# Optimization experiments

Measured on AMD Instinct MI355X. Metric: run time of the kernel, lower is better.

## Reference

```python
import jax, jax.numpy as jnp
import numpy as np
import math

DIM, H, Q_RANK, KV_RANK = 2048, 16, 768, 512
QK_STATIC, QK_ROT, V_DIM = 128, 64, 128
QK_TOTAL = QK_STATIC + QK_ROT
BS, SEQ = 2, 1024


def rmsnorm(x, scale, eps=1e-6):
    xf = x.astype(jnp.float32)
    return scale * (xf * jax.lax.rsqrt(jnp.mean(xf * xf, axis=-1, keepdims=True) + eps))


def half_rotate(x):
    h = x.shape[-1] // 2
    return jnp.concatenate([-x[..., h:], x[..., :h]], axis=-1)


def rope_tables(seq_len, dim):
    inv_freq = 1.0 / (10000.0 ** (jnp.arange(0, dim, 2, dtype=jnp.float32) / dim))
    freqs = jnp.arange(seq_len, dtype=jnp.float32)[:, None] * inv_freq[None, :]
    cos = jnp.concatenate([jnp.cos(freqs), jnp.cos(freqs)], axis=-1)  # (S, dim)
    sin = jnp.concatenate([jnp.sin(freqs), jnp.sin(freqs)], axis=-1)
    return cos, sin


def setup_inputs() -> dict:
    key = jax.random.key(0)
    ks = jax.random.split(key, 10)
    sc = lambda fan_in: 1.0 / math.sqrt(fan_in)
    x = jax.random.normal(ks[0], (BS, SEQ, DIM), dtype=jnp.float32)
    causal = jnp.where(jnp.tril(jnp.ones((SEQ, SEQ), dtype=bool)), 0.0, -1e9).astype(jnp.float32)
    mask = jnp.broadcast_to(causal[None], (BS, SEQ, SEQ))
    return {
        "x": x,
        "start_pos": 0,
        "mask": mask,
        "q_down_w": jax.random.normal(ks[1], (Q_RANK, DIM)) * sc(DIM),
        "q_down_b": jnp.zeros((Q_RANK,), jnp.float32),
        "q_norm_scale": jnp.ones((Q_RANK,), jnp.float32),
        "q_up_w": jax.random.normal(ks[2], (H * QK_TOTAL, Q_RANK)) * sc(Q_RANK),
        "q_up_b": jnp.zeros((H * QK_TOTAL,), jnp.float32),
        "kv_down_w": jax.random.normal(ks[3], (KV_RANK + QK_ROT, DIM)) * sc(DIM),
        "kv_down_b": jnp.zeros((KV_RANK + QK_ROT,), jnp.float32),
        "kv_norm_scale": jnp.ones((KV_RANK,), jnp.float32),
        "kv_up_w": jax.random.normal(ks[4], (H * (QK_STATIC + V_DIM), KV_RANK)) * sc(KV_RANK),
        "out_w": jax.random.normal(ks[5], (DIM, H * V_DIM)) * sc(H * V_DIM),
        "out_b": jnp.zeros((DIM,), jnp.float32),
    }


def reference(x, start_pos, mask, q_down_w, q_down_b, q_norm_scale, q_up_w, q_up_b,
              kv_down_w, kv_down_b, kv_norm_scale, kv_up_w, out_w, out_b):
    bs, seq_len, _ = x.shape
    # q path: down-proj -> RMSNorm -> up-proj
    q = rmsnorm(x @ q_down_w.T + q_down_b, q_norm_scale)
    q = (q @ q_up_w.T + q_up_b).reshape(bs, seq_len, H, QK_TOTAL)
    q_static, q_rot = q[..., :QK_STATIC], q[..., QK_STATIC:]
    # kv path: shared down-proj producing latent features + rotary key part
    kv = x @ kv_down_w.T + kv_down_b
    kv_feat, k_rot = kv[..., :KV_RANK], kv[..., KV_RANK:]
    # RoPE (original indexes positions 0..seq_len-1)
    cos, sin = rope_tables(seq_len, QK_ROT)
    q_rot = q_rot * cos[None, :, None, :] + half_rotate(q_rot) * sin[None, :, None, :]
    k_rot = k_rot * cos[None, :, :] + half_rotate(k_rot) * sin[None, :, :]  # (b, t, r)
    kv_normed = rmsnorm(kv_feat, kv_norm_scale)  # latent cache contents (b, t, c)
    # matrix absorption: fold kv_up key-weights into q
    w_k_abs = kv_up_w[: H * QK_STATIC, :].reshape(H, QK_STATIC, KV_RANK)
    w_v_abs = kv_up_w[-H * V_DIM :, :].reshape(H, V_DIM, KV_RANK)
    q_static_proj = jnp.einsum('bshd,hdc->bshc', q_static, w_k_abs)
    attn_scores = (jnp.einsum('bshc,btc->bsht', q_static_proj, kv_normed)
                   + jnp.einsum('bshr,btr->bsht', q_rot, k_rot)) / math.sqrt(QK_TOTAL)
    attn_scores = attn_scores + mask[:, :, None, :]
    attn_weights = jax.nn.softmax(attn_scores, axis=-1)
    # attend over latent features, then expand with absorbed value weights
    ctx_c = jnp.einsum('bsht,btc->bshc', attn_weights, kv_normed)
    ctx = jnp.einsum('bshc,hdc->bshd', ctx_c, w_v_abs)
    out = ctx.reshape(bs, seq_len, H * V_DIM) @ out_w.T + out_b
    return out
```

## Files before the change

kernel.cpp:

```cpp
#include <hip/hip_runtime.h>
#include <stdint.h>
#include <stddef.h>


typedef __attribute__((ext_vector_type(8))) short bf16x8;
typedef __attribute__((ext_vector_type(4))) float f32x4;

__device__ inline float b2f(unsigned short v){
    union { unsigned u; float f; } x; x.u = ((unsigned)v) << 16; return x.f;
}
__device__ inline unsigned short f2b(float f){
    union { float f; unsigned u; } x; x.f = f;
    unsigned r = x.u + 0x7fffu + ((x.u >> 16) & 1u);
    return (unsigned short)(r >> 16);
}

__device__ __forceinline__ void gl2lds16(const unsigned short* g, unsigned short* l){
    __builtin_amdgcn_global_load_lds(
        (__attribute__((address_space(1))) void*)const_cast<unsigned short*>(g),
        (__attribute__((address_space(3))) void*)l,
        16, 0, 0);
}

template<typename TC>
__global__ __launch_bounds__(256) void mfma_gemm_bt(
    const unsigned short* __restrict__ A, const unsigned short* __restrict__ B,
    const float* __restrict__ bias, TC* __restrict__ C,
    int M, int N, int K, int lda, int ldb, int ldc,
    int zdiv, long sA_hi, long sA_lo, long sB_hi, long sB_lo, long sC_hi, long sC_lo,
    float alpha, int causal)
{
    int z, bm, bn;
    if (causal & 4){ z = blockIdx.x; bm = blockIdx.y; bn = blockIdx.z; }
    else           { z = blockIdx.z; bm = blockIdx.y; bn = blockIdx.x; }
    int m0, n0;
    if (causal & 1){
        int i = bm;
        int mt = (int)((sqrtf(8.f * i + 1.f) - 1.f) * 0.5f);
        while ((mt + 1) * (mt + 2) / 2 <= i) ++mt;
        while (mt * (mt + 1) / 2 > i) --mt;
        n0 = (i - mt * (mt + 1) / 2) * 128;
        m0 = mt * 128;
    } else { m0 = bm * 128; n0 = bn * 128; }
    if (causal & 2) K = min(K, m0 + 128);

    __shared__ unsigned short As[3][4096];
    __shared__ unsigned short Bs[3][4096];
    const int zh = z / zdiv, zl = z % zdiv;
    A += (size_t)zh * sA_hi + (size_t)zl * sA_lo;
    B += (size_t)zh * sB_hi + (size_t)zl * sB_lo;
    C += (size_t)zh * sC_hi + (size_t)zl * sC_lo;

    const int tid = threadIdx.x, w = tid >> 6, lane = tid & 63;
    const int wm = w >> 1, wn = w & 1;

    const int srow = w * 32 + (lane >> 2);
    const int schunk = ((lane & 3) ^ ((lane >> 3) & 3)) * 8;
    const unsigned short* gA = A + (size_t)(m0 + srow) * lda + schunk;
    const unsigned short* gB = B + (size_t)(n0 + srow) * ldb + schunk;

    const int ktiles = K >> 5;
    auto stage = [&](int buf, int kt){
        const int k0 = kt << 5;
        gl2lds16(gA + k0,            &As[buf][w * 1024]);
        gl2lds16(gA + k0 + 16 * lda, &As[buf][w * 1024 + 512]);
        gl2lds16(gB + k0,            &Bs[buf][w * 1024]);
        gl2lds16(gB + k0 + 16 * ldb, &Bs[buf][w * 1024 + 512]);
    };
    stage(0, 0);
    if (ktiles > 1) stage(1, 1);

    f32x4 acc[4][4] = {};
    const int lm = lane & 15;
    const int kq = (((lane >> 4) ^ (lm >> 1)) & 3) * 8;

    int cur = 0;
    for (int kt = 0; kt < ktiles; ++kt){
        if (kt + 1 < ktiles) __builtin_amdgcn_s_waitcnt(0xF74);
        else                 __builtin_amdgcn_s_waitcnt(0xF70);
        __builtin_amdgcn_s_barrier();
        __asm__ volatile("" ::: "memory");
        if (kt + 2 < ktiles) stage(cur >= 1 ? cur - 1 : 2, kt + 2);
        bf16x8 af[4], bfr[4];
        #pragma unroll
        for (int i = 0; i < 4; ++i)
            af[i] = *(const bf16x8*)&As[cur][(wm * 64 + i * 16 + lm) * 32 + kq];
        #pragma unroll
        for (int j = 0; j < 4; ++j)
            bfr[j] = *(const bf16x8*)&Bs[cur][(wn * 64 + j * 16 + lm) * 32 + kq];
        #pragma unroll
        for (int i = 0; i < 4; ++i)
            #pragma unroll
            for (int j = 0; j < 4; ++j)
                acc[i][j] = __builtin_amdgcn_mfma_f32_16x16x32_bf16(af[i], bfr[j], acc[i][j], 0, 0, 0);
        __asm__ volatile("" ::: "memory");
        cur = (cur == 2) ? 0 : cur + 1;
    }

    #pragma unroll
    for (int i = 0; i < 4; ++i){
        const int m = m0 + wm * 64 + i * 16 + (lane >> 4) * 4;
        #pragma unroll
        for (int j = 0; j < 4; ++j){
            const int n = n0 + wn * 64 + j * 16 + lm;
            if (n < N){
                const float bb = bias ? bias[n] : 0.f;
                #pragma unroll
                for (int r = 0; r < 4; ++r){
                    float v = acc[i][j][r] * alpha + bb;
                    if ((causal & 1) && n > m + r) v = -1e9f;
                    if constexpr (sizeof(TC) == 2)
                        C[(size_t)(m + r) * ldc + n] = (TC)f2b(v);
                    else
                        C[(size_t)(m + r) * ldc + n] = (TC)v;
                }
            }
        }
    }
}

__global__ __launch_bounds__(256) void flash_attn(
    const unsigned short* __restrict__ qu,
    const unsigned short* __restrict__ khcat,
    const unsigned short* __restrict__ vhT,
    unsigned short* __restrict__ ctx)
{
    const int z = blockIdx.x;
    const int mt = 15 - (int)blockIdx.y;
    const int b = z >> 4, h = z & 15;
    const int m0 = mt * 64;
    const int nkt = (mt >> 1) + 1;

    __shared__ char smem[74240];
    unsigned short (*Qs)[4096] = (unsigned short (*)[4096])smem;
    unsigned short (*Ks)[8192] = (unsigned short (*)[8192])(smem + 24576);
    unsigned short* Ps = (unsigned short*)(smem + 24576);
    float* lrow = (float*)(smem + 73728);

    const unsigned short* kB = khcat + (size_t)z * 196608;
    const unsigned short* vB = vhT + (size_t)z * 131072;

    const int tid = threadIdx.x, w = tid >> 6, lane = tid & 63;
    const int wm = w >> 1, wn = w & 1;
    const int lm = lane & 15, g = lane >> 4;
    const int kq = g * 8;
    const int rs7 = lm & 7;

    if (tid < 128) lrow[tid] = 0.f;

    const int srow8 = lane >> 3;
    const int soff8 = ((lane & 7) ^ (lane >> 3)) * 8;
    const unsigned short* gQ = qu + (size_t)(b * 1024 + m0 + w * 16 + srow8) * 3072
                               + h * 192 + soff8;

    #pragma unroll
    for (int c = 0; c < 3; ++c){
        gl2lds16(gQ + c * 64,            &Qs[c][w * 1024]);
        gl2lds16(gQ + c * 64 + 8 * 3072, &Qs[c][w * 1024 + 512]);
    }

    f32x4 Oacc[2][4] = {};
    const float scl = 0.07216878364870322f;

    for (int kt = 0; kt < nkt; ++kt){
        bf16x8 vfr[4][4];
        #pragma unroll
        for (int j = 0; j < 4; ++j)
            #pragma unroll
            for (int kc = 0; kc < 4; ++kc)
                vfr[j][kc] = *(const bf16x8*)(vB + (size_t)(wn * 64 + j * 16 + lm) * 1024
                                              + kt * 128 + kc * 32 + kq);

        const unsigned short* gK = kB + (size_t)(kt * 128 + w * 32 + srow8) * 192 + soff8;
        auto stageK = [&](int buf, int c){
            const int k0 = c * 64;
            gl2lds16(gK + k0,            &Ks[buf][w * 2048]);
            gl2lds16(gK + k0 + 8 * 192,  &Ks[buf][w * 2048 + 512]);
            gl2lds16(gK + k0 + 16 * 192, &Ks[buf][w * 2048 + 1024]);
            gl2lds16(gK + k0 + 24 * 192, &Ks[buf][w * 2048 + 1536]);
        };
        stageK(0, 0);
        stageK(1, 1);

        f32x4 S[2][4] = {};
        #pragma unroll
        for (int c = 0; c < 3; ++c){
            if (c < 2) __builtin_amdgcn_s_waitcnt(0xF74);
            else       __builtin_amdgcn_s_waitcnt(0xF70);
            __builtin_amdgcn_s_barrier();
            __asm__ volatile("" ::: "memory");
            if (c == 0) stageK(2, 2);
            bf16x8 af[2][2], bfr[4][2];
            #pragma unroll
            for (int i = 0; i < 2; ++i)
                #pragma unroll
                for (int kk = 0; kk < 2; ++kk)
                    af[i][kk] = *(const bf16x8*)&Qs[c][(wm * 32 + i * 16 + lm) * 64
                                                       + (((kk * 4 + g) ^ rs7) * 8)];
            #pragma unroll
            for (int j = 0; j < 4; ++j)
                #pragma unroll
                for (int kk = 0; kk < 2; ++kk)
                    bfr[j][kk] = *(const bf16x8*)&Ks[c][(wn * 64 + j * 16 + lm) * 64
                                                        + (((kk * 4 + g) ^ rs7) * 8)];
            #pragma unroll
            for (int kk = 0; kk < 2; ++kk)
                #pragma unroll
                for (int i = 0; i < 2; ++i)
                    #pragma unroll
                    for (int j = 0; j < 4; ++j)
                        S[i][j] = __builtin_amdgcn_mfma_f32_16x16x32_bf16(af[i][kk], bfr[j][kk], S[i][j], 0, 0, 0);
            __asm__ volatile("" ::: "memory");
        }
        __syncthreads();

        const bool diag = (kt == (mt >> 1));
        #pragma unroll
        for (int i = 0; i < 2; ++i){
            float rs[4] = {0.f, 0.f, 0.f, 0.f};
            #pragma unroll
            for (int j = 0; j < 4; ++j){
                const int nloc = wn * 64 + j * 16 + lm;
                #pragma unroll
                for (int r = 0; r < 4; ++r){
                    const int mloc = wm * 32 + i * 16 + g * 4 + r;
                    float p = __expf(S[i][j][r] * scl);
                    if (diag && (kt * 128 + nloc) > (m0 + mloc)) p = 0.f;
                    rs[r] += p;
                    Ps[mloc * 136 + nloc] = f2b(p);
                }
            }
            #pragma unroll
            for (int r = 0; r < 4; ++r){
                rs[r] += __shfl_xor(rs[r], 1, 64);
                rs[r] += __shfl_xor(rs[r], 2, 64);
                rs[r] += __shfl_xor(rs[r], 4, 64);
                rs[r] += __shfl_xor(rs[r], 8, 64);
            }
            if (lm == 0){
                #pragma unroll
                for (int r = 0; r < 4; ++r)
                    lrow[wn * 64 + wm * 32 + i * 16 + g * 4 + r] += rs[r];
            }
        }
        __syncthreads();

        #pragma unroll
        for (int kc = 0; kc < 4; ++kc){
            bf16x8 pa[2];
            #pragma unroll
            for (int i = 0; i < 2; ++i)
                pa[i] = *(const bf16x8*)&Ps[(wm * 32 + i * 16 + lm) * 136 + kc * 32 + kq];
            #pragma unroll
            for (int i = 0; i < 2; ++i)
                #pragma unroll
                for (int j = 0; j < 4; ++j)
                    Oacc[i][j] = __builtin_amdgcn_mfma_f32_16x16x32_bf16(pa[i], vfr[j][kc], Oacc[i][j], 0, 0, 0);
        }
        __syncthreads();
    }

    unsigned short* cBase = ctx + ((size_t)(b * 1024 + m0)) * 2048 + h * 128;
    #pragma unroll
    for (int i = 0; i < 2; ++i){
        #pragma unroll
        for (int r = 0; r < 4; ++r){
            const int row = wm * 32 + i * 16 + g * 4 + r;
            const float inv = 1.f / (lrow[row] + lrow[64 + row]);
            #pragma unroll
            for (int j = 0; j < 4; ++j){
                const int col = wn * 64 + j * 16 + lm;
                cBase[(size_t)row * 2048 + col] = f2b(Oacc[i][j][r] * inv);
            }
        }
    }
}

__global__ __launch_bounds__(256) void cast_all(
    const float* __restrict__ s0, unsigned short* __restrict__ d0,
    const float* __restrict__ s1, unsigned short* __restrict__ d1,
    const float* __restrict__ s2, unsigned short* __restrict__ d2,
    const float* __restrict__ s3, unsigned short* __restrict__ d3,
    const float* __restrict__ s4, unsigned short* __restrict__ d4,
    const float* __restrict__ s5, unsigned short* __restrict__ d5)
{
    long i = (long)(blockIdx.x * 256 + threadIdx.x) * 4;
    const float* s; unsigned short* d; long off;
    if      (i <  4194304L){ s = s0; d = d0; off = i; }
    else if (i <  5767168L){ s = s1; d = d1; off = i -  4194304L; }
    else if (i <  8126464L){ s = s2; d = d2; off = i -  5767168L; }
    else if (i <  9306112L){ s = s3; d = d3; off = i -  8126464L; }
    else if (i < 11403264L){ s = s4; d = d4; off = i -  9306112L; }
    else                   { s = s5; d = d5; off = i - 11403264L; }
    float4 v = *(const float4*)(s + off);
    *(ushort4*)(d + off) = make_ushort4(f2b(v.x), f2b(v.y), f2b(v.z), f2b(v.w));
}

__global__ __launch_bounds__(256) void fused_down_post(
    const unsigned short* __restrict__ p,
    const float* __restrict__ q_down_b, const float* __restrict__ kv_down_b,
    const float* __restrict__ q_norm_s, const float* __restrict__ kv_norm_s,
    unsigned short* __restrict__ qn, unsigned short* __restrict__ kcat)
{
    __shared__ float row[1344];
    __shared__ float red[4];
    const int t = blockIdx.x, tid = threadIdx.x;
    const long S = 2752512L;
    const unsigned short* b0 = p + (size_t)t * 1344;
    for (int c = tid; c < 1344; c += 256){
        float v = b2f(b0[c]) + b2f(b0[c + S]) + b2f(b0[c + 2*S]) + b2f(b0[c + 3*S]);
        v += (c < 768) ? q_down_b[c] : kv_down_b[c - 768];
        row[c] = v;
    }
    __syncthreads();
    const int lane = tid & 63, w = tid >> 6;
    float ss = 0.f;
    for (int c = tid; c < 768; c += 256){ float v = row[c]; ss += v * v; }
    #pragma unroll
    for (int o = 32; o > 0; o >>= 1) ss += __shfl_xor(ss, o, 64);
    if (lane == 0) red[w] = ss;
    __syncthreads();
    const float inv1 = rsqrtf((red[0]+red[1]+red[2]+red[3]) / 768.f + 1e-6f);
    __syncthreads();
    ss = 0.f;
    for (int c = tid; c < 512; c += 256){ float v = row[768 + c]; ss += v * v; }
    #pragma unroll
    for (int o = 32; o > 0; o >>= 1) ss += __shfl_xor(ss, o, 64);
    if (lane == 0) red[w] = ss;
    __syncthreads();
    const float inv2 = rsqrtf((red[0]+red[1]+red[2]+red[3]) / 512.f + 1e-6f);
    for (int c = tid; c < 768; c += 256)
        qn[(size_t)t * 768 + c] = f2b(q_norm_s[c] * row[c] * inv1);
    for (int c = tid; c < 512; c += 256)
        kcat[(size_t)t * 576 + c] = f2b(kv_norm_s[c] * row[768 + c] * inv2);
    if (tid < 64){
        const int d = tid, s = t & 1023;
        float x  = row[1280 + d];
        float xp = (d < 32) ? -row[1280 + d + 32] : row[1280 + d - 32];
        float ang = (float)s * powf(10000.f, -(float)(2 * (d & 31)) / 64.f);
        kcat[(size_t)t * 576 + 512 + d] = f2b(x * cosf(ang) + xp * sinf(ang));
    }
}

__global__ __launch_bounds__(256) void reduce_out(
    const unsigned short* __restrict__ p, const float* __restrict__ bias,
    float* __restrict__ out)
{
    const long S = 4194304L;
    long i = (long)(blockIdx.x * 256 + threadIdx.x) * 4;
    ushort4 a = *(const ushort4*)(p + i);
    ushort4 b = *(const ushort4*)(p + i + S);
    float4 bb = *(const float4*)(bias + (i & 2047));
    float4 r = make_float4(b2f(a.x) + b2f(b.x) + bb.x, b2f(a.y) + b2f(b.y) + bb.y,
                           b2f(a.z) + b2f(b.z) + bb.z, b2f(a.w) + b2f(b.w) + bb.w);
    *(float4*)(out + i) = r;
}

__global__ __launch_bounds__(256) void rope_q_krot(
    unsigned short* __restrict__ qu,
    const unsigned short* __restrict__ kcat,
    unsigned short* __restrict__ khcat)
{
    long idx = (long)blockIdx.x * 256 + threadIdx.x;
    if (idx < 1048576L){
        const int d   = idx & 31;
        const int h   = (idx >> 5) & 15;
        const int tok = idx >> 9;
        const int s   = tok & 1023;
        unsigned short* base = qu + (size_t)tok * 3072 + h * 192 + 128;
        float x1 = b2f(base[d]), x2 = b2f(base[d + 32]);
        float ang = (float)s * powf(10000.f, -(float)d / 32.f);
        float c = cosf(ang), sn = sinf(ang);
        base[d]      = f2b(x1 * c - x2 * sn);
        base[d + 32] = f2b(x2 * c + x1 * sn);
    } else {
        idx -= 1048576L;
        const int d   = idx & 63;
        const int h   = (idx >> 6) & 15;
        const int tok = (int)(idx >> 10);
        const int bb  = tok >> 10, s = tok & 1023;
        khcat[((size_t)(bb * 16 + h) * 1024 + s) * 192 + 128 + d] =
            kcat[(size_t)tok * 576 + 512 + d];
    }
}

extern "C" void kernel_launch(void* const* d_in, const int* in_sizes, int n_in,
                              void* d_out, int out_size, void* d_ws, size_t ws_size,
                              hipStream_t stream)
{
    const float* x         = (const float*)d_in[0];
    const float* q_down_w  = (const float*)d_in[3];
    const float* q_down_b  = (const float*)d_in[4];
    const float* q_norm_s  = (const float*)d_in[5];
    const float* q_up_w    = (const float*)d_in[6];
    const float* q_up_b    = (const float*)d_in[7];
    const float* kv_down_w = (const float*)d_in[8];
    const float* kv_down_b = (const float*)d_in[9];
    const float* kv_norm_s = (const float*)d_in[10];
    const float* kv_up_w   = (const float*)d_in[11];
    const float* out_w     = (const float*)d_in[12];
    const float* out_b     = (const float*)d_in[13];
    float* out = (float*)d_out;

    char* ws = (char*)d_ws;
    unsigned short* kvuw  = (unsigned short*)(ws + 0);
    unsigned short* outw  = (unsigned short*)(ws + 4194304);
    unsigned short* kcat  = (unsigned short*)(ws + 12582912);
    unsigned short* vhT   = (unsigned short*)(ws + 14942208);
    unsigned short* khcat = (unsigned short*)(ws + 23330816);
    unsigned short* ctx   = (unsigned short*)(ws + 35913728);
    unsigned short* qu    = (unsigned short*)(ws + 44302336);
    unsigned short* qn    = (unsigned short*)(ws + 56885248);
    unsigned short* p_qkv = (unsigned short*)(ws + 60030976);
    unsigned short* p_out = (unsigned short*)(ws + 60030976);
    unsigned short* xb    = (unsigned short*)(ws + 82051072);
    unsigned short* qkdw  = (unsigned short*)(ws + 90439680);
    unsigned short* quw   = (unsigned short*)(ws + 96206848);

    dim3 blk(256);

    cast_all<<<15232, blk, 0, stream>>>(x, xb, q_down_w, qkdw, q_up_w, quw,
                                        kv_down_w, qkdw + 1572864, kv_up_w, kvuw, out_w, outw);

    mfma_gemm_bt<unsigned short><<<dim3(11, 16, 4), blk, 0, stream>>>(
        xb, qkdw, nullptr, p_qkv, 2048, 1344, 512, 2048, 2048, 1344,
        4, 0L, 512L, 0L, 512L, 0L, 2752512L, 1.0f, 0);
    fused_down_post<<<2048, blk, 0, stream>>>(p_qkv, q_down_b, kv_down_b,
                                              q_norm_s, kv_norm_s, qn, kcat);
    mfma_gemm_bt<unsigned short><<<dim3(24, 16, 1), blk, 0, stream>>>(
        qn, quw, q_up_b, qu, 2048, 3072, 768, 768, 768, 3072,
        1, 0, 0, 0, 0, 0, 0, 1.0f, 0);
    mfma_gemm_bt<unsigned short><<<dim3(32, 1, 8), blk, 0, stream>>>(
        kvuw + 1048576, kcat, nullptr, vhT, 128, 1024, 512, 512, 576, 1024,
        16, 0L, 65536L, 589824L, 0L, 2097152L, 131072L, 1.0f, 4);
    mfma_gemm_bt<unsigned short><<<dim3(32, 8, 1), blk, 0, stream>>>(
        kcat, kvuw, nullptr, khcat, 1024, 128, 512, 576, 512, 192,
        16, 589824L, 0L, 0L, 65536L, 3145728L, 196608L, 1.0f, 4);
    rope_q_krot<<<12288, blk, 0, stream>>>(qu, kcat, khcat);
    flash_attn<<<dim3(32, 16), blk, 0, stream>>>(qu, khcat, vhT, ctx);
    mfma_gemm_bt<unsigned short><<<dim3(16, 16, 2), blk, 0, stream>>>(
        ctx, outw, nullptr, p_out, 2048, 2048, 1024, 2048, 2048, 2048,
        2, 0L, 1024L, 0L, 1024L, 0L, 4194304L, 1.0f, 0);
    reduce_out<<<4096, blk, 0, stream>>>(p_out, out_b, out);
}
```

Baseline: 311.5 us.

## Remap attention blocks for causal load balance and prefetch K across tiles

```diff
diff --git a/kernel.cpp b/kernel.cpp
--- a/kernel.cpp
+++ b/kernel.cpp
@@ -125,11 +125,17 @@
     const unsigned short* __restrict__ vhT,
     unsigned short* __restrict__ ctx)
 {
-    const int z = blockIdx.x;
-    const int mt = 15 - (int)blockIdx.y;
+    const int t = blockIdx.x;
+    const int k15 = t & 15, kl = k15 & 7;
+    int v = (kl & 1) ? (1 + (kl >> 1)) : (8 - (kl >> 1));
+    if (k15 & 8) v = 9 - v;
+    if (t & 256) v = 9 - v;
+    const int o = ((t >> 4) & 15) * 2 + (k15 >> 3) + ((t >> 8) << 5);
+    const int mt = 2 * v - 2 + (o & 1);
+    const int z  = o >> 1;
     const int b = z >> 4, h = z & 15;
     const int m0 = mt * 64;
-    const int nkt = (mt >> 1) + 1;
+    const int nkt = v;
 
     __shared__ char smem[74240];
     unsigned short (*Qs)[4096] = (unsigned short (*)[4096])smem;
@@ -159,10 +165,23 @@
         gl2lds16(gQ + c * 64 + 8 * 3072, &Qs[c][w * 1024 + 512]);
     }
 
+    auto stageK = [&](int buf, int kt, int c){
+        const unsigned short* gK = kB + (size_t)(kt * 128 + w * 32 + srow8) * 192
+                                   + c * 64 + soff8;
+        gl2lds16(gK,            &Ks[buf][w * 2048]);
+        gl2lds16(gK + 8 * 192,  &Ks[buf][w * 2048 + 512]);
+        gl2lds16(gK + 16 * 192, &Ks[buf][w * 2048 + 1024]);
+        gl2lds16(gK + 24 * 192, &Ks[buf][w * 2048 + 1536]);
+    };
+    stageK(2, 0, 0);
+
     f32x4 Oacc[2][4] = {};
     const float scl = 0.07216878364870322f;
 
     for (int kt = 0; kt < nkt; ++kt){
+        stageK(0, kt, 1);
+        stageK(1, kt, 2);
+        __asm__ volatile("" ::: "memory");
         bf16x8 vfr[4][4];
         #pragma unroll
         for (int j = 0; j < 4; ++j)
@@ -170,26 +189,17 @@
             for (int kc = 0; kc < 4; ++kc)
                 vfr[j][kc] = *(const bf16x8*)(vB + (size_t)(wn * 64 + j * 16 + lm) * 1024
                                               + kt * 128 + kc * 32 + kq);
-
-        const unsigned short* gK = kB + (size_t)(kt * 128 + w * 32 + srow8) * 192 + soff8;
-        auto stageK = [&](int buf, int c){
-            const int k0 = c * 64;
-            gl2lds16(gK + k0,            &Ks[buf][w * 2048]);
-            gl2lds16(gK + k0 + 8 * 192,  &Ks[buf][w * 2048 + 512]);
-            gl2lds16(gK + k0 + 16 * 192, &Ks[buf][w * 2048 + 1024]);
-            gl2lds16(gK + k0 + 24 * 192, &Ks[buf][w * 2048 + 1536]);
-        };
-        stageK(0, 0);
-        stageK(1, 1);
+        __asm__ volatile("" ::: "memory");
 
         f32x4 S[2][4] = {};
         #pragma unroll
         for (int c = 0; c < 3; ++c){
-            if (c < 2) __builtin_amdgcn_s_waitcnt(0xF74);
-            else       __builtin_amdgcn_s_waitcnt(0xF70);
+            if      (c == 0) __builtin_amdgcn_s_waitcnt(0x4F78);
+            else if (c == 1) __builtin_amdgcn_s_waitcnt(0x4F74);
+            else             __builtin_amdgcn_s_waitcnt(0x4F70);
             __builtin_amdgcn_s_barrier();
             __asm__ volatile("" ::: "memory");
-            if (c == 0) stageK(2, 2);
+            const int bufc = (c == 0) ? 2 : (c - 1);
             bf16x8 af[2][2], bfr[4][2];
             #pragma unroll
             for (int i = 0; i < 2; ++i)
@@ -201,8 +211,9 @@
             for (int j = 0; j < 4; ++j)
                 #pragma unroll
                 for (int kk = 0; kk < 2; ++kk)
-                    bfr[j][kk] = *(const bf16x8*)&Ks[c][(wn * 64 + j * 16 + lm) * 64
-                                                        + (((kk * 4 + g) ^ rs7) * 8)];
+                    bfr[j][kk] = *(const bf16x8*)&Ks[bufc][(wn * 64 + j * 16 + lm) * 64
+                                                           + (((kk * 4 + g) ^ rs7) * 8)];
+            __builtin_amdgcn_s_setprio(1);
             #pragma unroll
             for (int kk = 0; kk < 2; ++kk)
                 #pragma unroll
@@ -210,9 +221,13 @@
                     #pragma unroll
                     for (int j = 0; j < 4; ++j)
                         S[i][j] = __builtin_amdgcn_mfma_f32_16x16x32_bf16(af[i][kk], bfr[j][kk], S[i][j], 0, 0, 0);
+            __builtin_amdgcn_s_setprio(0);
             __asm__ volatile("" ::: "memory");
         }
-        __syncthreads();
+        __builtin_amdgcn_s_waitcnt(0xC07F);
+        __builtin_amdgcn_s_barrier();
+        __asm__ volatile("" ::: "memory");
+        if (kt + 1 < nkt) stageK(2, kt + 1, 0);
 
         const bool diag = (kt == (mt >> 1));
         #pragma unroll
@@ -243,21 +258,31 @@
                     lrow[wn * 64 + wm * 32 + i * 16 + g * 4 + r] += rs[r];
             }
         }
-        __syncthreads();
-
+        __asm__ volatile("" ::: "memory");
+        __builtin_amdgcn_s_waitcnt(0xC07F);
+        __builtin_amdgcn_s_barrier();
+        __asm__ volatile("" ::: "memory");
+
+        if (kt + 1 < nkt) __builtin_amdgcn_s_waitcnt(0xF74);
+        else              __builtin_amdgcn_s_waitcnt(0xF70);
         #pragma unroll
         for (int kc = 0; kc < 4; ++kc){
             bf16x8 pa[2];
             #pragma unroll
             for (int i = 0; i < 2; ++i)
                 pa[i] = *(const bf16x8*)&Ps[(wm * 32 + i * 16 + lm) * 136 + kc * 32 + kq];
+            __builtin_amdgcn_s_setprio(1);
             #pragma unroll
             for (int i = 0; i < 2; ++i)
                 #pragma unroll
                 for (int j = 0; j < 4; ++j)
                     Oacc[i][j] = __builtin_amdgcn_mfma_f32_16x16x32_bf16(pa[i], vfr[j][kc], Oacc[i][j], 0, 0, 0);
+            __builtin_amdgcn_s_setprio(0);
         }
-        __syncthreads();
+        __asm__ volatile("" ::: "memory");
+        __builtin_amdgcn_s_waitcnt(0xC07F);
+        __builtin_amdgcn_s_barrier();
+        __asm__ volatile("" ::: "memory");
     }
 
     unsigned short* cBase = ctx + ((size_t)(b * 1024 + m0)) * 2048 + h * 128;
@@ -437,7 +462,7 @@
         kcat, kvuw, nullptr, khcat, 1024, 128, 512, 576, 512, 192,
         16, 589824L, 0L, 0L, 65536L, 3145728L, 196608L, 1.0f, 4);
     rope_q_krot<<<12288, blk, 0, stream>>>(qu, kcat, khcat);
-    flash_attn<<<dim3(32, 16), blk, 0, stream>>>(qu, khcat, vhT, ctx);
+    flash_attn<<<dim3(512), blk, 0, stream>>>(qu, khcat, vhT, ctx);
     mfma_gemm_bt<unsigned short><<<dim3(16, 16, 2), blk, 0, stream>>>(
         ctx, outw, nullptr, p_out, 2048, 2048, 1024, 2048, 2048, 2048,
         2, 0L, 1024L, 0L, 1024L, 0L, 4194304L, 1.0f, 0);
```

Result: faster. 301.2 us (-3.3%).
